# Kernel tuning notes

Hardware: AMD Instinct MI355X
Metric: run time of the kernel (lower is better)

Reference implementation:

```python
import jax, jax.numpy as jnp
import numpy as np

SOBEL_X = jnp.array([[-1., 0., 1.], [-2., 0., 2.], [-1., 0., 1.]], dtype=jnp.float32).reshape(1, 1, 3, 3)
SOBEL_Y = jnp.array([[-1., -2., -1.], [0., 0., 0.], [1., 2., 1.]], dtype=jnp.float32).reshape(1, 1, 3, 3)


def _gray(x):
    # x: (B, 3, H, W) -> (B, 1, H, W)
    if x.shape[1] == 3:
        return 0.299 * x[:, 0:1] + 0.587 * x[:, 1:2] + 0.114 * x[:, 2:3]
    return x


def _edges(g):
    # g: (B, 1, H, W); 3x3 Sobel convs with padding 1 (cross-correlation, like torch conv2d)
    dn = ('NCHW', 'OIHW', 'NCHW')
    ex = jax.lax.conv_general_dilated(g, SOBEL_X, (1, 1), ((1, 1), (1, 1)), dimension_numbers=dn)
    ey = jax.lax.conv_general_dilated(g, SOBEL_Y, (1, 1), ((1, 1), (1, 1)), dimension_numbers=dn)
    return jnp.sqrt(ex * ex + ey * ey)


def setup_inputs() -> dict:
    key = jax.random.key(0)
    k1, k2 = jax.random.split(key)
    pred = jax.random.normal(k1, (32, 3, 512, 512), dtype=jnp.float32)
    target = jax.random.normal(k2, (32, 3, 512, 512), dtype=jnp.float32)
    return {"pred": pred, "target": target}


def reference(pred, target):
    pred_edges = _edges(_gray(pred))
    target_edges = _edges(_gray(target))
    return jnp.mean(jnp.abs(pred_edges - target_edges))
```

## Files before the change

kernel.cpp:

```cpp
#include <hip/hip_runtime.h>


#define BATCH 32
#define HH 512
#define WW 512
#define TX 64
#define TY 32
#define HALO_W (TX + 2)
#define HALO_H (TY + 2)
#define HALO_N (HALO_W * HALO_H)

__global__ void zero_out_kernel(float* out) { out[0] = 0.0f; }

__global__ __launch_bounds__(256) void edge_loss_kernel(
    const float* __restrict__ pred,
    const float* __restrict__ target,
    float* __restrict__ out)
{
    __shared__ float gp[HALO_N];
    __shared__ float gt[HALO_N];

    const int tid = threadIdx.x;
    const int x0 = blockIdx.x * TX;
    const int y0 = blockIdx.y * TY;
    const int b  = blockIdx.z;

    const size_t img = (size_t)HH * WW;
    const float* pbase = pred   + (size_t)b * 3 * img;
    const float* tbase = target + (size_t)b * 3 * img;

    for (int idx = tid; idx < HALO_N; idx += 256) {
        const int ly = idx / HALO_W;
        const int lx = idx - ly * HALO_W;
        const int gy = y0 - 1 + ly;
        const int gx = x0 - 1 + lx;
        float vp = 0.0f, vt = 0.0f;
        if (gy >= 0 && gy < HH && gx >= 0 && gx < WW) {
            const int o = gy * WW + gx;
            vp = 0.299f * pbase[o] + 0.587f * pbase[o + img] + 0.114f * pbase[o + 2 * img];
            vt = 0.299f * tbase[o] + 0.587f * tbase[o + img] + 0.114f * tbase[o + 2 * img];
        }
        gp[idx] = vp;
        gt[idx] = vt;
    }
    __syncthreads();

    const int tx = tid & 63;
    const int ty = tid >> 6;
    float lsum = 0.0f;

    #pragma unroll
    for (int i = 0; i < TY / 4; ++i) {
        const int ry = ty + 4 * i;
        const float* cp = &gp[ry * HALO_W + tx];
        const float* ct = &gt[ry * HALO_W + tx];

        float p00 = cp[0],          p01 = cp[1],              p02 = cp[2];
        float p10 = cp[HALO_W],                               p12 = cp[HALO_W + 2];
        float p20 = cp[2*HALO_W],   p21 = cp[2*HALO_W + 1],   p22 = cp[2*HALO_W + 2];
        float ex = (p02 - p00) + 2.0f * (p12 - p10) + (p22 - p20);
        float ey = (p20 - p00) + 2.0f * (p21 - p01) + (p22 - p02);
        float ep = sqrtf(ex * ex + ey * ey);

        float t00 = ct[0],          t01 = ct[1],              t02 = ct[2];
        float t10 = ct[HALO_W],                               t12 = ct[HALO_W + 2];
        float t20 = ct[2*HALO_W],   t21 = ct[2*HALO_W + 1],   t22 = ct[2*HALO_W + 2];
        float fx = (t02 - t00) + 2.0f * (t12 - t10) + (t22 - t20);
        float fy = (t20 - t00) + 2.0f * (t21 - t01) + (t22 - t02);
        float et = sqrtf(fx * fx + fy * fy);

        lsum += fabsf(ep - et);
    }

    #pragma unroll
    for (int off = 32; off > 0; off >>= 1)
        lsum += __shfl_down(lsum, off, 64);

    __shared__ float wsum[4];
    if ((tid & 63) == 0) wsum[ty] = lsum;
    __syncthreads();
    if (tid == 0) {
        const float s = wsum[0] + wsum[1] + wsum[2] + wsum[3];
        const float inv_n = 1.0f / ((float)BATCH * HH * WW);
        atomicAdd(out, s * inv_n);
    }
}

extern "C" void kernel_launch(void* const* d_in, const int* in_sizes, int n_in,
                              void* d_out, int out_size, void* d_ws, size_t ws_size,
                              hipStream_t stream) {
    const float* pred   = (const float*)d_in[0];
    const float* target = (const float*)d_in[1];
    float* out = (float*)d_out;

    zero_out_kernel<<<1, 1, 0, stream>>>(out);

    dim3 grid(WW / TX, HH / TY, BATCH);
    edge_loss_kernel<<<grid, 256, 0, stream>>>(pred, target, out);
}
```

Before: 231.8 us.

## Replace shared-memory halo tiles with register sliding-window row streaming

Removes the shared-memory halo tile and sync. Each thread now handles 4 columns across a 16-row band, loading rows with float4 vector loads and keeping a 3-row rolling window in registers, so each gray row is computed once per thread column group. Full-width 512-column rows per block remove horizontal halo recomputation, but neighbouring float4s are loaded redundantly for the left/right edges and register pressure rises. The grid becomes 16x32 blocks, which lowers parallelism.

```diff
diff --git a/kernel.cpp b/kernel.cpp
--- a/kernel.cpp
+++ b/kernel.cpp
@@ -4,82 +4,136 @@
 #define BATCH 32
 #define HH 512
 #define WW 512
-#define TX 64
-#define TY 32
-#define HALO_W (TX + 2)
-#define HALO_H (TY + 2)
-#define HALO_N (HALO_W * HALO_H)
+#define RR 16
+#define BANDS 2
+#define TILE_H (RR * BANDS)
 
 __global__ void zero_out_kernel(float* out) { out[0] = 0.0f; }
 
-__global__ __launch_bounds__(256) void edge_loss_kernel(
+struct GRow { float v[6]; };
+
+__device__ __forceinline__ void zero_row(GRow& g) {
+    #pragma unroll
+    for (int i = 0; i < 6; ++i) g.v[i] = 0.0f;
+}
+
+__device__ __forceinline__ float grayf(float r, float g, float b) {
+    return 0.299f * r + 0.587f * g + 0.114f * b;
+}
+
+__device__ __forceinline__ void gray_row(
+    const float* __restrict__ pbase, const float* __restrict__ tbase,
+    int row, int x, bool okL, bool okR, GRow& gp, GRow& gt)
+{
+    const size_t img = (size_t)HH * WW;
+    const float4 z4 = make_float4(0.f, 0.f, 0.f, 0.f);
+    const float* pA = pbase + (size_t)row * WW + x;
+    const float* tA = tbase + (size_t)row * WW + x;
+
+    float4 prL = okL ? *(const float4*)(pA - 4)           : z4;
+    float4 prM =       *(const float4*)(pA);
+    float4 prR = okR ? *(const float4*)(pA + 4)           : z4;
+    float4 pgL = okL ? *(const float4*)(pA + img - 4)     : z4;
+    float4 pgM =       *(const float4*)(pA + img);
+    float4 pgR = okR ? *(const float4*)(pA + img + 4)     : z4;
+    float4 pbL = okL ? *(const float4*)(pA + 2 * img - 4) : z4;
+    float4 pbM =       *(const float4*)(pA + 2 * img);
+    float4 pbR = okR ? *(const float4*)(pA + 2 * img + 4) : z4;
+    float4 trL = okL ? *(const float4*)(tA - 4)           : z4;
+    float4 trM =       *(const float4*)(tA);
+    float4 trR = okR ? *(const float4*)(tA + 4)           : z4;
+    float4 tgL = okL ? *(const float4*)(tA + img - 4)     : z4;
+    float4 tgM =       *(const float4*)(tA + img);
+    float4 tgR = okR ? *(const float4*)(tA + img + 4)     : z4;
+    float4 tbL = okL ? *(const float4*)(tA + 2 * img - 4) : z4;
+    float4 tbM =       *(const float4*)(tA + 2 * img);
+    float4 tbR = okR ? *(const float4*)(tA + 2 * img + 4) : z4;
+
+    gp.v[0] = grayf(prL.w, pgL.w, pbL.w);
+    gp.v[1] = grayf(prM.x, pgM.x, pbM.x);
+    gp.v[2] = grayf(prM.y, pgM.y, pbM.y);
+    gp.v[3] = grayf(prM.z, pgM.z, pbM.z);
+    gp.v[4] = grayf(prM.w, pgM.w, pbM.w);
+    gp.v[5] = grayf(prR.x, pgR.x, pbR.x);
+
+    gt.v[0] = grayf(trL.w, tgL.w, tbL.w);
+    gt.v[1] = grayf(trM.x, tgM.x, tbM.x);
+    gt.v[2] = grayf(trM.y, tgM.y, tbM.y);
+    gt.v[3] = grayf(trM.z, tgM.z, tbM.z);
+    gt.v[4] = grayf(trM.w, tgM.w, tbM.w);
+    gt.v[5] = grayf(trR.x, tgR.x, tbR.x);
+}
+
+__device__ __forceinline__ float sobel4(
+    const GRow& pm1, const GRow& pc0, const GRow& pp1,
+    const GRow& tm1, const GRow& tc0, const GRow& tp1)
+{
+    float s = 0.0f;
+    #pragma unroll
+    for (int i = 0; i < 4; ++i) {
+        float ex = (pm1.v[i+2] - pm1.v[i]) + 2.0f * (pc0.v[i+2] - pc0.v[i])
+                 + (pp1.v[i+2] - pp1.v[i]);
+        float ey = (pp1.v[i] + 2.0f * pp1.v[i+1] + pp1.v[i+2])
+                 - (pm1.v[i] + 2.0f * pm1.v[i+1] + pm1.v[i+2]);
+        float ep = sqrtf(ex * ex + ey * ey);
+
+        float fx = (tm1.v[i+2] - tm1.v[i]) + 2.0f * (tc0.v[i+2] - tc0.v[i])
+                 + (tp1.v[i+2] - tp1.v[i]);
+        float fy = (tp1.v[i] + 2.0f * tp1.v[i+1] + tp1.v[i+2])
+                 - (tm1.v[i] + 2.0f * tm1.v[i+1] + tm1.v[i+2]);
+        float et = sqrtf(fx * fx + fy * fy);
+
+        s += fabsf(ep - et);
+    }
+    return s;
+}
+
+__global__ __launch_bounds__(256, 2) void edge_loss_kernel(
     const float* __restrict__ pred,
     const float* __restrict__ target,
     float* __restrict__ out)
 {
-    __shared__ float gp[HALO_N];
-    __shared__ float gt[HALO_N];
+    const int t    = threadIdx.x;
+    const int tx   = t & 127;
+    const int band = t >> 7;
+    const int x    = tx * 4;
+    const int b      = blockIdx.y;
+    const int yStart = blockIdx.x * TILE_H + band * RR;
 
-    const int tid = threadIdx.x;
-    const int x0 = blockIdx.x * TX;
-    const int y0 = blockIdx.y * TY;
-    const int b  = blockIdx.z;
+    const bool okL = (tx > 0);
+    const bool okR = (tx < 127);
 
     const size_t img = (size_t)HH * WW;
     const float* pbase = pred   + (size_t)b * 3 * img;
     const float* tbase = target + (size_t)b * 3 * img;
 
-    for (int idx = tid; idx < HALO_N; idx += 256) {
-        const int ly = idx / HALO_W;
-        const int lx = idx - ly * HALO_W;
-        const int gy = y0 - 1 + ly;
-        const int gx = x0 - 1 + lx;
-        float vp = 0.0f, vt = 0.0f;
-        if (gy >= 0 && gy < HH && gx >= 0 && gx < WW) {
-            const int o = gy * WW + gx;
-            vp = 0.299f * pbase[o] + 0.587f * pbase[o + img] + 0.114f * pbase[o + 2 * img];
-            vt = 0.299f * tbase[o] + 0.587f * tbase[o + img] + 0.114f * tbase[o + 2 * img];
-        }
-        gp[idx] = vp;
-        gt[idx] = vt;
-    }
-    __syncthreads();
+    GRow pm1, pc0, tm1, tc0;
+    if (yStart - 1 >= 0) gray_row(pbase, tbase, yStart - 1, x, okL, okR, pm1, tm1);
+    else { zero_row(pm1); zero_row(tm1); }
+    gray_row(pbase, tbase, yStart, x, okL, okR, pc0, tc0);
 
-    const int tx = tid & 63;
-    const int ty = tid >> 6;
-    float lsum = 0.0f;
+    float acc = 0.0f;
+    #pragma unroll
+    for (int k = 0; k < RR; ++k) {
+        const int rnext = yStart + k + 1;
+        GRow pp1, tp1;
+        if (rnext < HH) gray_row(pbase, tbase, rnext, x, okL, okR, pp1, tp1);
+        else { zero_row(pp1); zero_row(tp1); }
 
-    #pragma unroll
-    for (int i = 0; i < TY / 4; ++i) {
-        const int ry = ty + 4 * i;
-        const float* cp = &gp[ry * HALO_W + tx];
-        const float* ct = &gt[ry * HALO_W + tx];
+        acc += sobel4(pm1, pc0, pp1, tm1, tc0, tp1);
 
-        float p00 = cp[0],          p01 = cp[1],              p02 = cp[2];
-        float p10 = cp[HALO_W],                               p12 = cp[HALO_W + 2];
-        float p20 = cp[2*HALO_W],   p21 = cp[2*HALO_W + 1],   p22 = cp[2*HALO_W + 2];
-        float ex = (p02 - p00) + 2.0f * (p12 - p10) + (p22 - p20);
-        float ey = (p20 - p00) + 2.0f * (p21 - p01) + (p22 - p02);
-        float ep = sqrtf(ex * ex + ey * ey);
-
-        float t00 = ct[0],          t01 = ct[1],              t02 = ct[2];
-        float t10 = ct[HALO_W],                               t12 = ct[HALO_W + 2];
-        float t20 = ct[2*HALO_W],   t21 = ct[2*HALO_W + 1],   t22 = ct[2*HALO_W + 2];
-        float fx = (t02 - t00) + 2.0f * (t12 - t10) + (t22 - t20);
-        float fy = (t20 - t00) + 2.0f * (t21 - t01) + (t22 - t02);
-        float et = sqrtf(fx * fx + fy * fy);
-
-        lsum += fabsf(ep - et);
+        pm1 = pc0; pc0 = pp1;
+        tm1 = tc0; tc0 = tp1;
     }
 
     #pragma unroll
     for (int off = 32; off > 0; off >>= 1)
-        lsum += __shfl_down(lsum, off, 64);
+        acc += __shfl_down(acc, off, 64);
 
     __shared__ float wsum[4];
-    if ((tid & 63) == 0) wsum[ty] = lsum;
+    if ((t & 63) == 0) wsum[t >> 6] = acc;
     __syncthreads();
-    if (tid == 0) {
+    if (t == 0) {
         const float s = wsum[0] + wsum[1] + wsum[2] + wsum[3];
         const float inv_n = 1.0f / ((float)BATCH * HH * WW);
         atomicAdd(out, s * inv_n);
@@ -95,6 +149,6 @@
 
     zero_out_kernel<<<1, 1, 0, stream>>>(out);
 
-    dim3 grid(WW / TX, HH / TY, BATCH);
+    dim3 grid(HH / TILE_H, BATCH);
     edge_loss_kernel<<<grid, 256, 0, stream>>>(pred, target, out);
 }
```

New measurement: 271.7 us. 1.17x slower.

## Stage RGB tiles into LDS via async global_load_lds, then compute grayscale

Applied to the files above, without the earlier changes.

Replaces per-thread scalar global loads with 16-byte direct global-to-LDS async loads of aligned float4 RGB halo tiles for both images. A separate pass then converts them to grayscale in shared memory before the Sobel stage. The tile height is halved to 16, which increases the block count, and border tiles are zero-filled for padding. This aims to widen memory transactions and cut per-thread address arithmetic, at the cost of extra LDS use, an extra barrier, and loading a wider 4-column halo on each side.

```diff
diff --git a/kernel.cpp b/kernel.cpp
--- a/kernel.cpp
+++ b/kernel.cpp
@@ -4,85 +4,128 @@
 #define BATCH 32
 #define HH 512
 #define WW 512
-#define TX 64
-#define TY 32
-#define HALO_W (TX + 2)
-#define HALO_H (TY + 2)
-#define HALO_N (HALO_W * HALO_H)
+#define PLANE (HH * WW)
+
+#define TLX 64
+#define TLY 16
+#define HR (TLY + 2)
+#define HC4 18
+#define HCF (HC4 * 4)
+#define NPL 6
+#define RGB_SLOTS (NPL * HR * HC4)
+#define GRAYS (2 * HR * HCF)
 
 __global__ void zero_out_kernel(float* out) { out[0] = 0.0f; }
+
+__device__ __forceinline__ void async_load16(const float* g, float* l) {
+    __builtin_amdgcn_global_load_lds(
+        (const __attribute__((address_space(1))) unsigned int*)g,
+        (__attribute__((address_space(3))) unsigned int*)l,
+        16, 0, 0);
+}
 
 __global__ __launch_bounds__(256) void edge_loss_kernel(
     const float* __restrict__ pred,
     const float* __restrict__ target,
     float* __restrict__ out)
 {
-    __shared__ float gp[HALO_N];
-    __shared__ float gt[HALO_N];
+    __shared__ float rgbs[RGB_SLOTS * 4];
+    __shared__ float grys[GRAYS];
+    __shared__ float wsum[4];
 
-    const int tid = threadIdx.x;
-    const int x0 = blockIdx.x * TX;
-    const int y0 = blockIdx.y * TY;
+    const unsigned t    = threadIdx.x;
+    const unsigned lane = t & 63u;
+    const unsigned w    = t >> 6;
+    const int x0 = blockIdx.x * TLX;
+    const int y0 = blockIdx.y * TLY;
     const int b  = blockIdx.z;
 
-    const size_t img = (size_t)HH * WW;
-    const float* pbase = pred   + (size_t)b * 3 * img;
-    const float* tbase = target + (size_t)b * 3 * img;
+    const float* pb = pred   + (size_t)b * 3 * PLANE;
+    const float* tb = target + (size_t)b * 3 * PLANE;
 
-    for (int idx = tid; idx < HALO_N; idx += 256) {
-        const int ly = idx / HALO_W;
-        const int lx = idx - ly * HALO_W;
-        const int gy = y0 - 1 + ly;
-        const int gx = x0 - 1 + lx;
-        float vp = 0.0f, vt = 0.0f;
-        if (gy >= 0 && gy < HH && gx >= 0 && gx < WW) {
-            const int o = gy * WW + gx;
-            vp = 0.299f * pbase[o] + 0.587f * pbase[o + img] + 0.114f * pbase[o + 2 * img];
-            vt = 0.299f * tbase[o] + 0.587f * tbase[o + img] + 0.114f * tbase[o + 2 * img];
+    if (x0 == 0 || y0 == 0 || x0 + TLX == WW || y0 + TLY == HH) {
+        #pragma unroll
+        for (unsigned k = 0; k < 8; ++k) {
+            const unsigned s = t + k * 256u;
+            if (s < RGB_SLOTS) {
+                const unsigned rem = s % (HR * HC4);
+                const int r   = rem / HC4;
+                const int c   = rem % HC4;
+                const int gy  = y0 - 1 + r;
+                const int gxf = x0 - 4 + 4 * c;
+                if (gy < 0 || gy >= HH || gxf < 0 || gxf > WW - 4) {
+                    *(float4*)(rgbs + (size_t)s * 4) =
+                        make_float4(0.f, 0.f, 0.f, 0.f);
+                }
+            }
         }
-        gp[idx] = vp;
-        gt[idx] = vt;
+    }
+
+    #pragma unroll
+    for (unsigned k = 0; k < 8; ++k) {
+        const unsigned sbase = k * 256u + w * 64u;
+        const unsigned s = sbase + lane;
+        float* ldst = rgbs + (size_t)sbase * 4;
+        if (s < RGB_SLOTS) {
+            const unsigned p   = s / (HR * HC4);
+            const unsigned rem = s % (HR * HC4);
+            const int r   = rem / HC4;
+            const int c   = rem % HC4;
+            const int gy  = y0 - 1 + r;
+            const int gxf = x0 - 4 + 4 * c;
+            if (gy >= 0 && gy < HH && gxf >= 0 && gxf <= WW - 4) {
+                const float* src = (p < 3 ? pb : tb)
+                                 + (size_t)(p % 3) * PLANE
+                                 + (size_t)gy * WW + gxf;
+                async_load16(src, ldst);
+            }
+        }
     }
     __syncthreads();
 
-    const int tx = tid & 63;
-    const int ty = tid >> 6;
-    float lsum = 0.0f;
+    #pragma unroll
+    for (unsigned k = 0; k < 11; ++k) {
+        const unsigned g = t + k * 256u;
+        if (g < GRAYS) {
+            const unsigned i    = g / (HR * HCF);
+            const unsigned rrem = g - i * (HR * HCF);
+            const unsigned base = i * 3 * (HR * HCF) + rrem;
+            const float R = rgbs[base];
+            const float G = rgbs[base + HR * HCF];
+            const float B = rgbs[base + 2 * HR * HCF];
+            grys[g] = 0.299f * R + 0.587f * G + 0.114f * B;
+        }
+    }
+    __syncthreads();
 
+    float acc = 0.0f;
     #pragma unroll
-    for (int i = 0; i < TY / 4; ++i) {
-        const int ry = ty + 4 * i;
-        const float* cp = &gp[ry * HALO_W + tx];
-        const float* ct = &gt[ry * HALO_W + tx];
-
-        float p00 = cp[0],          p01 = cp[1],              p02 = cp[2];
-        float p10 = cp[HALO_W],                               p12 = cp[HALO_W + 2];
-        float p20 = cp[2*HALO_W],   p21 = cp[2*HALO_W + 1],   p22 = cp[2*HALO_W + 2];
-        float ex = (p02 - p00) + 2.0f * (p12 - p10) + (p22 - p20);
-        float ey = (p20 - p00) + 2.0f * (p21 - p01) + (p22 - p02);
-        float ep = sqrtf(ex * ex + ey * ey);
-
-        float t00 = ct[0],          t01 = ct[1],              t02 = ct[2];
-        float t10 = ct[HALO_W],                               t12 = ct[HALO_W + 2];
-        float t20 = ct[2*HALO_W],   t21 = ct[2*HALO_W + 1],   t22 = ct[2*HALO_W + 2];
-        float fx = (t02 - t00) + 2.0f * (t12 - t10) + (t22 - t20);
-        float fy = (t20 - t00) + 2.0f * (t21 - t01) + (t22 - t02);
-        float et = sqrtf(fx * fx + fy * fy);
-
-        lsum += fabsf(ep - et);
+    for (unsigned k = 0; k < 4; ++k) {
+        const unsigned ry = w + 4 * k;
+        float mag[2];
+        #pragma unroll
+        for (int i = 0; i < 2; ++i) {
+            const float* gm = grys + (i * HR + ry    ) * HCF + lane + 3;
+            const float* gc = grys + (i * HR + ry + 1) * HCF + lane + 3;
+            const float* gq = grys + (i * HR + ry + 2) * HCF + lane + 3;
+            const float m0 = gm[0], m1 = gm[1], m2 = gm[2];
+            const float c0 = gc[0],              c2 = gc[2];
+            const float q0 = gq[0], q1 = gq[1], q2 = gq[2];
+            const float ex = (m2 - m0) + 2.0f * (c2 - c0) + (q2 - q0);
+            const float ey = (q0 + 2.0f * q1 + q2) - (m0 + 2.0f * m1 + m2);
+            mag[i] = sqrtf(ex * ex + ey * ey);
+        }
+        acc += fabsf(mag[0] - mag[1]);
     }
 
     #pragma unroll
     for (int off = 32; off > 0; off >>= 1)
-        lsum += __shfl_down(lsum, off, 64);
-
-    __shared__ float wsum[4];
-    if ((tid & 63) == 0) wsum[ty] = lsum;
+        acc += __shfl_down(acc, off, 64);
+    if (lane == 0) wsum[w] = acc;
     __syncthreads();
-    if (tid == 0) {
+    if (t == 0) {
         const float s = wsum[0] + wsum[1] + wsum[2] + wsum[3];
-        const float inv_n = 1.0f / ((float)BATCH * HH * WW);
-        atomicAdd(out, s * inv_n);
+        atomicAdd(out, s * (1.0f / 8388608.0f));
     }
 }
 
@@ -95,6 +138,6 @@
 
     zero_out_kernel<<<1, 1, 0, stream>>>(out);
 
-    dim3 grid(WW / TX, HH / TY, BATCH);
+    dim3 grid(WW / TLX, HH / TLY, BATCH);
     edge_loss_kernel<<<grid, 256, 0, stream>>>(pred, target, out);
 }
```

Result: slower. 260.6 us (+12.5%).
